# Kernel optimization log

Hardware: AMD Instinct MI355X
Metric: run time of the kernel (lower is better)

Reference implementation:

```python
import jax, jax.numpy as jnp
import numpy as np

B, T, EMB, HEAD = 8, 2048, 1024, 1024

def setup_inputs() -> dict:
    key = jax.random.key(0)
    k1, k2, k3, k4 = jax.random.split(key, 4)
    s = 1.0 / np.sqrt(EMB)
    return {
        "x": jax.random.normal(k1, (B, T, EMB), dtype=jnp.float32),
        "Wq": jax.random.normal(k2, (HEAD, EMB), dtype=jnp.float32) * s,
        "Wk": jax.random.normal(k3, (HEAD, EMB), dtype=jnp.float32) * s,
        "Wv": jax.random.normal(k4, (HEAD, EMB), dtype=jnp.float32) * s,
    }

def reference(x, Wq, Wk, Wv):
    # Bias-free projections; torch Linear weight is [out, in] -> contract on last dim.
    q = jnp.einsum('btc,hc->bth', x, Wq)  # [B,T,HEAD]
    k = jnp.einsum('btc,hc->bth', x, Wk)
    v = jnp.einsum('btc,hc->bth', x, Wv)
    C = x.shape[-1]
    scale = jnp.asarray(C, x.dtype) ** -0.5  # NOTE: scales by emb dim C, as in source
    wei = jnp.einsum('bth,bsh->bts', q, k) * scale  # [B,T,T]
    Tn = x.shape[1]
    causal = jnp.tril(jnp.ones((Tn, Tn), dtype=bool))
    wei = jnp.where(causal, wei, -jnp.inf)
    wei = jax.nn.softmax(wei, axis=-1)
    # dropout omitted (eval mode / deterministic reference)
    out = jnp.einsum('bts,bsh->bth', wei, v)  # [B,T,HEAD]
    return out
```

## Files before the change

### kernel.cpp

```cpp
#include <hip/hip_runtime.h>

typedef unsigned short u16;
typedef short short8 __attribute__((ext_vector_type(8)));
typedef float f32x4 __attribute__((ext_vector_type(4)));
typedef unsigned long long u64;

#define WS_K_OFF    33554432ULL
#define WS_PTRI     67108864ULL
#define WS_PART     104857600ULL
#define WS_NEED     105447424ULL
#define W2_K        33554432ULL
#define W2_VT       67108864ULL
#define W2_PTRI     100663296ULL
#define W2_PART     138412032ULL
#define W2_NEED     139001856ULL

__device__ __forceinline__ u16 f2bf(float f) {
    union { float f; unsigned u; } c; c.f = f;
    unsigned r = c.u + 0x7fffu + ((c.u >> 16) & 1u);
    return (u16)(r >> 16);
}
__device__ __forceinline__ float bf2f(u16 h) {
    union { unsigned u; float f; } c; c.u = ((unsigned)h) << 16; return c.f;
}
__device__ __forceinline__ void gll16(const u16* g, u16* l) {
    __builtin_amdgcn_global_load_lds(
        (const __attribute__((address_space(1))) void*)g,
        (__attribute__((address_space(3))) void*)l, 16, 0, 0);
}

template<int AMODE>
__device__ __forceinline__ void gemm_pipe(
    const u16* __restrict__ A, int lda,
    const u16* __restrict__ B, int ldb,
    int m0, int n0, int nk, u16* lds, f32x4 acc[8][4])
{
    const int tid  = threadIdx.x;
    const int lane = tid & 63;
    const int w    = tid >> 6;
    const int wm   = w >> 2, wn = w & 3;
    const int kg   = lane >> 4, l15 = lane & 15;
    const int r0   = w * 32 + (lane >> 2);
    const int s0   = (lane & 3) ^ ((r0 >> 1) & 3);

    const int ldA = AMODE ? 256 : lda;
    const u16* Ar0 = A + (size_t)(m0 + r0) * ldA + s0 * 8;
    const u16* Ar1 = Ar0 + 16 * ldA;
    const u16* Br0 = B + (size_t)(n0 + r0) * ldb + s0 * 8;
    const u16* Br1 = Br0 + 16 * ldb;

    auto aoff = [&](int t) -> int {
        return AMODE ? ((t >> 3) * 65536 + (t & 7) * 32) : t * 32;
    };
    auto STAGE = [&](int t) {
        const int ao = aoff(t), bo = t * 32, buf = (t & 3) * 16384;
        u16* dA = lds + buf + w * 1024;
        u16* dB = lds + buf + 8192 + w * 1024;
        gll16(Ar0 + ao, dA);
        gll16(Ar1 + ao, dA + 512);
        gll16(Br0 + bo, dB);
        gll16(Br1 + bo, dB + 512);
    };
    auto LDA8 = [&](short8* fa, int t) {
        const u16* h = lds + (t & 3) * 16384 + wm * 4096;
        #pragma unroll
        for (int mt = 0; mt < 8; ++mt) {
            const int row = mt * 16 + l15;
            fa[mt] = *reinterpret_cast<const short8*>(
                h + row * 32 + ((kg ^ ((row >> 1) & 3)) << 3));
        }
    };
    auto LDB4 = [&](short8* fb, int t) {
        const u16* h = lds + (t & 3) * 16384 + 8192 + wn * 2048;
        #pragma unroll
        for (int nt = 0; nt < 4; ++nt) {
            const int row = nt * 16 + l15;
            fb[nt] = *reinterpret_cast<const short8*>(
                h + row * 32 + ((kg ^ ((row >> 1) & 3)) << 3));
        }
    };
    auto MFMA32 = [&](short8* fa, short8* fb) {
        __builtin_amdgcn_s_setprio(1);
        #pragma unroll
        for (int mt = 0; mt < 8; ++mt)
            #pragma unroll
            for (int nt = 0; nt < 4; ++nt)
                acc[mt][nt] = __builtin_amdgcn_mfma_f32_16x16x32_bf16(
                    fa[mt], fb[nt], acc[mt][nt], 0, 0, 0);
        __builtin_amdgcn_s_setprio(0);
    };

    STAGE(0); STAGE(1); STAGE(2);
    asm volatile("s_waitcnt vmcnt(4)" ::: "memory");
    __builtin_amdgcn_s_barrier();

    short8 faA[8], faB[8], fb[4];
    LDA8(faA, 0);

    for (int t = 0; t < nk; t += 2) {
        LDB4(fb, t);
        LDA8(faB, t + 1);
        if (t + 3 < nk) STAGE(t + 3);
        MFMA32(faA, fb);
        if (t + 3 < nk) asm volatile("s_waitcnt vmcnt(4)" ::: "memory");
        else            asm volatile("s_waitcnt vmcnt(0)" ::: "memory");
        __builtin_amdgcn_s_barrier();

        LDB4(fb, t + 1);
        if (t + 2 < nk) LDA8(faA, t + 2);
        if (t + 4 < nk) STAGE(t + 4);
        MFMA32(faB, fb);
        if (t + 4 < nk) asm volatile("s_waitcnt vmcnt(4)" ::: "memory");
        else            asm volatile("s_waitcnt vmcnt(0)" ::: "memory");
        __builtin_amdgcn_s_barrier();
    }
}

__global__ __launch_bounds__(256) void cvt_bf16(
    const float* __restrict__ x,
    const float* __restrict__ Wq,
    const float* __restrict__ Wk,
    const float* __restrict__ Wv,
    u16* __restrict__ dst)
{
    const size_t e = ((size_t)blockIdx.x * 256 + threadIdx.x) * 8;
    const float* src;
    if (e < (size_t)16777216) {
        src = x + e;
    } else {
        size_t j = e - 16777216;
        int z = (int)(j >> 20);
        const float* Wz = (z == 0) ? Wq : (z == 1) ? Wk : Wv;
        src = Wz + (j & 1048575);
    }
    float4 a = *reinterpret_cast<const float4*>(src);
    float4 b = *reinterpret_cast<const float4*>(src + 4);
    short8 v;
    v[0] = (short)f2bf(a.x); v[1] = (short)f2bf(a.y);
    v[2] = (short)f2bf(a.z); v[3] = (short)f2bf(a.w);
    v[4] = (short)f2bf(b.x); v[5] = (short)f2bf(b.y);
    v[6] = (short)f2bf(b.z); v[7] = (short)f2bf(b.w);
    *reinterpret_cast<short8*>(dst + e) = v;
}

__global__ __launch_bounds__(512, 2) void qkv_pipe(
    const u16* __restrict__ xb, const u16* __restrict__ Wb,
    u16* __restrict__ Qo, u16* __restrict__ Ko, u16* __restrict__ VTo, int zbase)
{
    __shared__ u16 L[65536];
    const int tid = threadIdx.x, lane = tid & 63, w = tid >> 6;
    const int wm = w >> 2, wn = w & 3, kg = lane >> 4, l15 = lane & 15;
    const int m0 = blockIdx.x * 256, n0 = blockIdx.y * 256;
    const int z = blockIdx.z + zbase;

    const f32x4 z4 = {0.f, 0.f, 0.f, 0.f};
    f32x4 acc[8][4];
    #pragma unroll
    for (int i = 0; i < 8; ++i)
        #pragma unroll
        for (int j = 0; j < 4; ++j) acc[i][j] = z4;

    gemm_pipe<0>(xb, 1024, Wb + (size_t)z * 1048576, 1024, m0, n0, 32, L, acc);

    if (z < 2) {
        u16* O = (z == 0) ? Qo : Ko;
        #pragma unroll
        for (int mt = 0; mt < 8; ++mt) {
            const int row0 = m0 + wm * 128 + mt * 16 + kg * 4;
            #pragma unroll
            for (int nt = 0; nt < 4; ++nt) {
                const int col = n0 + wn * 64 + nt * 16 + l15;
                #pragma unroll
                for (int r = 0; r < 4; ++r)
                    O[(size_t)(row0 + r) * 1024 + col] = f2bf(acc[mt][nt][r]);
            }
        }
    } else {
        const int b    = m0 >> 11;
        const int mloc = m0 & 2047;
        const int t8   = (tid & 31) * 8;
        const int hh   = tid >> 5;
        #pragma unroll
        for (int half = 0; half < 2; ++half) {
            if ((wn >> 1) == half) {
                const int hb = (wn & 1) * 64;
                #pragma unroll
                for (int mt = 0; mt < 8; ++mt) {
                    const int tl = wm * 128 + mt * 16 + kg * 4;
                    #pragma unroll
                    for (int nt = 0; nt < 4; ++nt) {
                        const int hl = hb + nt * 16 + l15;
                        u64 pk = (u64)f2bf(acc[mt][nt][0])
                               | ((u64)f2bf(acc[mt][nt][1]) << 16)
                               | ((u64)f2bf(acc[mt][nt][2]) << 32)
                               | ((u64)f2bf(acc[mt][nt][3]) << 48);
                        *reinterpret_cast<u64*>(&L[hl * 264 + tl]) = pk;
                    }
                }
            }
            __syncthreads();
            #pragma unroll
            for (int p = 0; p < 8; ++p) {
                const int hl = p * 16 + hh;
                short8 v = *reinterpret_cast<const short8*>(&L[hl * 264 + t8]);
                *reinterpret_cast<short8*>(
                    &VTo[((size_t)b * 1024 + n0 + half * 128 + hl) * 2048 + mloc + t8]) = v;
            }
            __syncthreads();
        }
    }
}

template<int AMODE>
__device__ __forceinline__ void gemm_tri128(
    const u16* __restrict__ A, int lda,
    const u16* __restrict__ B, int ldb, int nk, u16* L, f32x4 acc[4][4])
{
    const int tid = threadIdx.x, lane = tid & 63, w = tid >> 6;
    const int wm = w >> 1, wn = w & 1, kg = lane >> 4, l15 = lane & 15;

    const int rA = w * 32 + (lane >> 2);
    const int sA = (lane & 3) ^ ((rA >> 1) & 3);
    const int rB = w * 16 + (lane >> 2);
    const int sB = (lane & 3) ^ ((rB >> 1) & 3);
    const int ldA = AMODE ? 256 : lda;
    const u16* Ar0 = A + (size_t)rA * ldA + sA * 8;
    const u16* Ar1 = Ar0 + 16 * ldA;
    const u16* Br0 = B + (size_t)rB * ldb + sB * 8;

    auto aoff = [&](int t) -> int {
        return AMODE ? ((t >> 3) * 65536 + (t & 7) * 32) : t * 32;
    };
    auto STAGE = [&](int t) {
        u16* d = L + (t % 3) * 12288;
        gll16(Ar0 + aoff(t), d + w * 1024);
        gll16(Ar1 + aoff(t), d + w * 1024 + 512);
        gll16(Br0 + t * 32,  d + 8192 + w * 512);
    };
    auto LDA4 = [&](short8* fa, int t) {
        const u16* h = L + (t % 3) * 12288;
        #pragma unroll
        for (int mt = 0; mt < 4; ++mt) {
            const int row = wm * 64 + mt * 16 + l15;
            fa[mt] = *reinterpret_cast<const short8*>(
                h + row * 32 + ((kg ^ ((row >> 1) & 3)) << 3));
        }
    };
    auto LDB4 = [&](short8* fb, int t) {
        const u16* h = L + (t % 3) * 12288 + 8192;
        #pragma unroll
        for (int nt = 0; nt < 4; ++nt) {
            const int row = wn * 64 + nt * 16 + l15;
            fb[nt] = *reinterpret_cast<const short8*>(
                h + row * 32 + ((kg ^ ((row >> 1) & 3)) << 3));
        }
    };

    STAGE(0); STAGE(1);
    asm volatile("s_waitcnt vmcnt(3)" ::: "memory");
    __builtin_amdgcn_s_barrier();

    short8 fa[4], fb[4];
    for (int t = 0; t < nk; ++t) {
        LDA4(fa, t);
        LDB4(fb, t);
        if (t + 2 < nk) STAGE(t + 2);
        __builtin_amdgcn_s_setprio(1);
        #pragma unroll
        for (int mt = 0; mt < 4; ++mt)
            #pragma unroll
            for (int nt = 0; nt < 4; ++nt)
                acc[mt][nt] = __builtin_amdgcn_mfma_f32_16x16x32_bf16(
                    fa[mt], fb[nt], acc[mt][nt], 0, 0, 0);
        __builtin_amdgcn_s_setprio(0);
        if (t + 2 < nk) asm volatile("s_waitcnt vmcnt(3)" ::: "memory");
        else            asm volatile("s_waitcnt vmcnt(0)" ::: "memory");
        __builtin_amdgcn_s_barrier();
    }
}

__global__ __launch_bounds__(512, 4) void sp128(
    const u16* __restrict__ Q, const u16* __restrict__ K,
    u16* __restrict__ Ptri, float* __restrict__ part)
{
    __shared__ u16 L[36864];
    int jj = blockIdx.x;
    const int b = jj / 72;
    int r = jj - b * 72;
    int qb = 0;
    while (r >= 2 * qb + 2) { r -= 2 * qb + 2; ++qb; }
    const int kb = r;

    const int tid = threadIdx.x, lane = tid & 63, w = tid >> 6;
    const int wm = w >> 1, wn = w & 1, kg = lane >> 4, l15 = lane & 15;

    const f32x4 z4 = {0.f, 0.f, 0.f, 0.f};
    f32x4 acc[4][4];
    #pragma unroll
    for (int a_ = 0; a_ < 4; ++a_)
        #pragma unroll
        for (int j = 0; j < 4; ++j) acc[a_][j] = z4;

    gemm_tri128<0>(Q + (size_t)(b * 2048 + qb * 256) * 1024, 1024,
                   K + (size_t)(b * 2048 + kb * 128) * 1024, 1024,
                   32, L, acc);

    u16* Pt = Ptri + ((size_t)b * 36 + (qb * (qb + 1)) / 2 + (kb >> 1)) * 65536
                   + (kb & 1) * 128;
    float* psum = (float*)L;
    #pragma unroll
    for (int mt = 0; mt < 4; ++mt) {
        #pragma unroll
        for (int rr = 0; rr < 4; ++rr) {
            const int lt = wm * 64 + mt * 16 + kg * 4 + rr;
            const int gt = qb * 256 + lt;
            float ps = 0.f;
            #pragma unroll
            for (int nt = 0; nt < 4; ++nt) {
                const int lcol = wn * 64 + nt * 16 + l15;
                const int gs = kb * 128 + lcol;
                const float p = (gs <= gt) ? __expf(acc[mt][nt][rr] * 0.03125f) : 0.f;
                ps += p;
                Pt[(size_t)lt * 256 + lcol] = f2bf(p);
            }
            #pragma unroll
            for (int d = 1; d < 16; d <<= 1) ps += __shfl_xor(ps, d, 64);
            if (l15 == 0) psum[lt * 2 + wn] = ps;
        }
    }
    __syncthreads();
    if (tid < 256) {
        const float s = psum[tid * 2] + psum[tid * 2 + 1];
        part[(size_t)b * 18432 + (qb * qb + qb) * 256 + tid * (2 * qb + 2) + kb] = s;
    }
}

__global__ __launch_bounds__(512, 2) void sp_old(
    const u16* __restrict__ Q, const u16* __restrict__ K, u16* __restrict__ P)
{
    const int qb = blockIdx.x, kb = blockIdx.y, b = blockIdx.z;
    if (kb > qb) return;
    __shared__ u16 L[65536];
    const int tid = threadIdx.x, lane = tid & 63, w = tid >> 6;
    const int wm = w >> 2, wn = w & 3, kg = lane >> 4, l15 = lane & 15;

    const f32x4 z4 = {0.f, 0.f, 0.f, 0.f};
    f32x4 acc[8][4];
    #pragma unroll
    for (int i = 0; i < 8; ++i)
        #pragma unroll
        for (int j = 0; j < 4; ++j) acc[i][j] = z4;

    gemm_pipe<0>(Q, 1024, K, 1024, b * 2048 + qb * 256, b * 2048 + kb * 256, 32, L, acc);

    u16* Pb = P + (size_t)b * 2048 * 2048;
    #pragma unroll
    for (int mt = 0; mt < 8; ++mt) {
        const int trow0 = qb * 256 + wm * 128 + mt * 16 + kg * 4;
        #pragma unroll
        for (int nt = 0; nt < 4; ++nt) {
            const int scol = kb * 256 + wn * 64 + nt * 16 + l15;
            #pragma unroll
            for (int r = 0; r < 4; ++r) {
                const int trow = trow0 + r;
                const float p = (scol <= trow) ? __expf(acc[mt][nt][r] * 0.03125f) : 0.f;
                Pb[(size_t)trow * 2048 + scol] = f2bf(p);
            }
        }
    }
}

__global__ __launch_bounds__(512, 4) void pv128(
    const u16* __restrict__ Ptri, const u16* __restrict__ VT,
    const float* __restrict__ part, float* __restrict__ out)
{
    __shared__ u16 L[36864];
    const int i = blockIdx.x;
    const int c = i >> 7;
    const int j = (i >> 1) & 63;
    const int s = i & 1;
    const int q  = s ? c : 7 - c;
    const int b  = j >> 3;
    const int nb = j & 7;
    const int nk = (q + 1) * 8;

    const int tid = threadIdx.x, lane = tid & 63, w = tid >> 6;
    const int wm = w >> 1, wn = w & 1, kg = lane >> 4, l15 = lane & 15;

    const f32x4 z4 = {0.f, 0.f, 0.f, 0.f};
    f32x4 acc[4][4];
    #pragma unroll
    for (int a_ = 0; a_ < 4; ++a_)
        #pragma unroll
        for (int jx = 0; jx < 4; ++jx) acc[a_][jx] = z4;

    gemm_tri128<1>(Ptri + ((size_t)b * 36 + (q * (q + 1)) / 2) * 65536, 256,
                   VT + ((size_t)b * 1024 + nb * 128) * 2048, 2048,
                   nk, L, acc);

    float* Lf = (float*)L;
    if (tid < 256) {
        const int nkb = 2 * q + 2;
        const float* pp = part + (size_t)b * 18432 + (q * q + q) * 256 + tid * nkb;
        float sum = 0.f;
        for (int kb = 0; kb < nkb; ++kb) sum += pp[kb];
        Lf[tid] = 1.f / sum;
    }
    __syncthreads();

    #pragma unroll
    for (int mt = 0; mt < 4; ++mt) {
        const int lt0 = wm * 64 + mt * 16 + kg * 4;
        const size_t grow0 = (size_t)b * 2048 + q * 256 + lt0;
        float rs[4];
        #pragma unroll
        for (int r = 0; r < 4; ++r) rs[r] = Lf[lt0 + r];
        #pragma unroll
        for (int nt = 0; nt < 4; ++nt) {
            const int col = nb * 128 + wn * 64 + nt * 16 + l15;
            #pragma unroll
            for (int r = 0; r < 4; ++r)
                out[(grow0 + r) * 1024 + col] = acc[mt][nt][r] * rs[r];
        }
    }
}

__global__ __launch_bounds__(512, 2) void pv_old(
    const u16* __restrict__ P, const u16* __restrict__ VT, float* __restrict__ Of)
{
    const int b = blockIdx.x >> 3, qblk = blockIdx.x & 7;
    const int nb = blockIdx.y;
    const int nk = (qblk + 1) * 8;
    __shared__ u16 L[65536];
    const int tid = threadIdx.x, lane = tid & 63, w = tid >> 6;
    const int wm = w >> 2, wn = w & 3, kg = lane >> 4, l15 = lane & 15;

    const f32x4 z4 = {0.f, 0.f, 0.f, 0.f};
    f32x4 acc[8][4];
    #pragma unroll
    for (int i = 0; i < 8; ++i)
        #pragma unroll
        for (int j = 0; j < 4; ++j) acc[i][j] = z4;

    gemm_pipe<0>(P + (size_t)b * 2048 * 2048, 2048,
                 VT + (size_t)b * 1024 * 2048, 2048,
                 qblk * 256, nb * 256, nk, L, acc);

    #pragma unroll
    for (int mt = 0; mt < 8; ++mt) {
        const int trow0 = qblk * 256 + wm * 128 + mt * 16 + kg * 4;
        #pragma unroll
        for (int nt = 0; nt < 4; ++nt) {
            const int col = nb * 256 + wn * 64 + nt * 16 + l15;
            #pragma unroll
            for (int r = 0; r < 4; ++r)
                Of[((size_t)b * 2048 + trow0 + r) * 1024 + col] = acc[mt][nt][r];
        }
    }
}

__global__ __launch_bounds__(256) void finalize(
    const u16* __restrict__ P, const float* __restrict__ Of, float* __restrict__ out)
{
    const int row = blockIdx.x;
    const int tid = threadIdx.x;
    const int b = row >> 11, t = row & 2047;
    const int len = ((t >> 8) + 1) * 256;
    const u16* prow = P + ((size_t)b * 2048 + t) * 2048;

    float s = 0.f;
    const int i = tid * 8;
    if (i < len) {
        short8 v = *reinterpret_cast<const short8*>(prow + i);
        #pragma unroll
        for (int j = 0; j < 8; ++j) s += bf2f((u16)v[j]);
    }
    #pragma unroll
    for (int d = 1; d < 64; d <<= 1) s += __shfl_xor(s, d, 64);

    __shared__ float red[4];
    if ((tid & 63) == 0) red[tid >> 6] = s;
    __syncthreads();
    const float rinv = 1.f / (red[0] + red[1] + red[2] + red[3]);

    const size_t o = (size_t)row * 1024 + tid * 4;
    f32x4 v = *reinterpret_cast<const f32x4*>(Of + o);
    v[0] *= rinv; v[1] *= rinv; v[2] *= rinv; v[3] *= rinv;
    *reinterpret_cast<f32x4*>(out + o) = v;
}

extern "C" void kernel_launch(void* const* d_in, const int* in_sizes, int n_in,
                              void* d_out, int out_size, void* d_ws, size_t ws_size,
                              hipStream_t stream) {
    const float* x  = (const float*)d_in[0];
    const float* Wq = (const float*)d_in[1];
    const float* Wk = (const float*)d_in[2];
    const float* Wv = (const float*)d_in[3];

    u16* xb = (u16*)d_out;
    u16* Wb = xb + (size_t)16777216;

    cvt_bf16<<<dim3(9728), 256, 0, stream>>>(x, Wq, Wk, Wv, xb);

    if (ws_size >= W2_NEED) {
        u16*   Qb   = (u16*)d_ws;
        u16*   Kb   = (u16*)((char*)d_ws + W2_K);
        u16*   VTb  = (u16*)((char*)d_ws + W2_VT);
        u16*   Pt   = (u16*)((char*)d_ws + W2_PTRI);
        float* part = (float*)((char*)d_ws + W2_PART);

        qkv_pipe<<<dim3(64, 4, 3), 512, 0, stream>>>(xb, Wb, Qb, Kb, VTb, 0);
        sp128<<<dim3(576), 512, 0, stream>>>(Qb, Kb, Pt, part);
        pv128<<<dim3(512), 512, 0, stream>>>(Pt, VTb, part, (float*)d_out);
    } else if (ws_size >= WS_NEED) {
        u16*   Qb   = (u16*)d_ws;
        u16*   Kb   = (u16*)((char*)d_ws + WS_K_OFF);
        u16*   Pt   = (u16*)((char*)d_ws + WS_PTRI);
        float* part = (float*)((char*)d_ws + WS_PART);
        u16*   VTb  = Qb;

        qkv_pipe<<<dim3(64, 4, 2), 512, 0, stream>>>(xb, Wb, Qb, Kb, Qb, 0);
        sp128<<<dim3(576), 512, 0, stream>>>(Qb, Kb, Pt, part);
        qkv_pipe<<<dim3(64, 4, 1), 512, 0, stream>>>(xb, Wb, Qb, Kb, VTb, 2);
        pv128<<<dim3(512), 512, 0, stream>>>(Pt, VTb, part, (float*)d_out);
    } else {
        u16* Qb  = (u16*)d_ws;
        u16* Kb  = Qb + (size_t)16384 * 1024;
        u16* VTb = Kb + (size_t)16384 * 1024;
        float* Of = (float*)d_ws;
        u16* Pb = (u16*)d_out;

        qkv_pipe<<<dim3(64, 4, 3), 512, 0, stream>>>(xb, Wb, Qb, Kb, VTb, 0);
        sp_old<<<dim3(8, 8, 8), 512, 0, stream>>>(Qb, Kb, Pb);
        pv_old<<<dim3(64, 4), 512, 0, stream>>>(Pb, VTb, Of);
        finalize<<<dim3(16384), 256, 0, stream>>>(Pb, Of, (float*)d_out);
    }
}
```

Baseline: 254.6 us.

## Tile causal score kernel at 128x128 blocks to skip masked upper tiles

Replaces the 256x128 score kernel with a 128x128-tile kernel that uses 256 threads and enumerates only lower-triangular 128-row blocks (136 per batch instead of 72 256-row pairs). The intent is to skip the fully masked quarter tiles that the old 256-row tiling computed, and to give the scheduler more, smaller blocks. The row-sum partials layout changes to per-128-row blocks and the PV kernel's normalization read is updated to match. The trade-off is smaller tiles with less data reuse and a different pipeline wait count.

```diff
diff --git a/kernel.cpp b/kernel.cpp
--- a/kernel.cpp
+++ b/kernel.cpp
@@ -279,21 +279,28 @@
     }
 }
 
-__global__ __launch_bounds__(512, 4) void sp128(
+__global__ __launch_bounds__(256, 3) void sp64k(
     const u16* __restrict__ Q, const u16* __restrict__ K,
     u16* __restrict__ Ptri, float* __restrict__ part)
 {
-    __shared__ u16 L[36864];
+    __shared__ u16 L[24576];
     int jj = blockIdx.x;
-    const int b = jj / 72;
-    int r = jj - b * 72;
-    int qb = 0;
-    while (r >= 2 * qb + 2) { r -= 2 * qb + 2; ++qb; }
+    const int b = jj / 136;
+    int r = jj - b * 136;
+    int q128 = 0;
+    while (r >= q128 + 1) { r -= q128 + 1; ++q128; }
     const int kb = r;
 
     const int tid = threadIdx.x, lane = tid & 63, w = tid >> 6;
     const int wm = w >> 1, wn = w & 1, kg = lane >> 4, l15 = lane & 15;
 
+    const int r0 = tid >> 2;
+    const int s0 = (tid & 3) ^ ((r0 >> 1) & 3);
+    const u16* Ar0 = Q + (size_t)(b * 2048 + q128 * 128 + r0) * 1024 + s0 * 8;
+    const u16* Ar1 = Ar0 + (size_t)64 * 1024;
+    const u16* Br0 = K + (size_t)(b * 2048 + kb * 128 + r0) * 1024 + s0 * 8;
+    const u16* Br1 = Br0 + (size_t)64 * 1024;
+
     const f32x4 z4 = {0.f, 0.f, 0.f, 0.f};
     f32x4 acc[4][4];
     #pragma unroll
@@ -301,19 +308,65 @@
         #pragma unroll
         for (int j = 0; j < 4; ++j) acc[a_][j] = z4;
 
-    gemm_tri128<0>(Q + (size_t)(b * 2048 + qb * 256) * 1024, 1024,
-                   K + (size_t)(b * 2048 + kb * 128) * 1024, 1024,
-                   32, L, acc);
-
-    u16* Pt = Ptri + ((size_t)b * 36 + (qb * (qb + 1)) / 2 + (kb >> 1)) * 65536
-                   + (kb & 1) * 128;
+    auto STAGE = [&](int t) {
+        u16* d = L + (t % 3) * 8192;
+        gll16(Ar0 + t * 32, d + w * 512);
+        gll16(Ar1 + t * 32, d + 2048 + w * 512);
+        gll16(Br0 + t * 32, d + 4096 + w * 512);
+        gll16(Br1 + t * 32, d + 4096 + 2048 + w * 512);
+    };
+    auto LDA4 = [&](short8* fa, int t) {
+        const u16* h = L + (t % 3) * 8192;
+        #pragma unroll
+        for (int mt = 0; mt < 4; ++mt) {
+            const int row = wm * 64 + mt * 16 + l15;
+            fa[mt] = *reinterpret_cast<const short8*>(
+                h + row * 32 + ((kg ^ ((row >> 1) & 3)) << 3));
+        }
+    };
+    auto LDB4 = [&](short8* fb, int t) {
+        const u16* h = L + (t % 3) * 8192 + 4096;
+        #pragma unroll
+        for (int nt = 0; nt < 4; ++nt) {
+            const int row = wn * 64 + nt * 16 + l15;
+            fb[nt] = *reinterpret_cast<const short8*>(
+                h + row * 32 + ((kg ^ ((row >> 1) & 3)) << 3));
+        }
+    };
+
+    const int nk = 32;
+    STAGE(0); STAGE(1);
+    asm volatile("s_waitcnt vmcnt(4)" ::: "memory");
+    __builtin_amdgcn_s_barrier();
+
+    short8 fa[4], fb[4];
+    for (int t = 0; t < nk; ++t) {
+        LDA4(fa, t);
+        LDB4(fb, t);
+        if (t + 2 < nk) STAGE(t + 2);
+        __builtin_amdgcn_s_setprio(1);
+        #pragma unroll
+        for (int mt = 0; mt < 4; ++mt)
+            #pragma unroll
+            for (int nt = 0; nt < 4; ++nt)
+                acc[mt][nt] = __builtin_amdgcn_mfma_f32_16x16x32_bf16(
+                    fa[mt], fb[nt], acc[mt][nt], 0, 0, 0);
+        __builtin_amdgcn_s_setprio(0);
+        if (t + 2 < nk) asm volatile("s_waitcnt vmcnt(4)" ::: "memory");
+        else            asm volatile("s_waitcnt vmcnt(0)" ::: "memory");
+        __builtin_amdgcn_s_barrier();
+    }
+
+    const int q256 = q128 >> 1, kb256 = kb >> 1;
+    u16* Pt = Ptri + ((size_t)b * 36 + (q256 * (q256 + 1)) / 2 + kb256) * 65536
+                   + (size_t)(q128 & 1) * 128 * 256 + (kb & 1) * 128;
     float* psum = (float*)L;
     #pragma unroll
     for (int mt = 0; mt < 4; ++mt) {
         #pragma unroll
         for (int rr = 0; rr < 4; ++rr) {
             const int lt = wm * 64 + mt * 16 + kg * 4 + rr;
-            const int gt = qb * 256 + lt;
+            const int gt = q128 * 128 + lt;
             float ps = 0.f;
             #pragma unroll
             for (int nt = 0; nt < 4; ++nt) {
@@ -329,9 +382,10 @@
         }
     }
     __syncthreads();
-    if (tid < 256) {
+    if (tid < 128) {
         const float s = psum[tid * 2] + psum[tid * 2 + 1];
-        part[(size_t)b * 18432 + (qb * qb + qb) * 256 + tid * (2 * qb + 2) + kb] = s;
+        part[(size_t)b * 17408 + (size_t)(q128 * (q128 + 1) / 2) * 128
+             + tid * (q128 + 1) + kb] = s;
     }
 }
 
@@ -400,10 +454,13 @@
 
     float* Lf = (float*)L;
     if (tid < 256) {
-        const int nkb = 2 * q + 2;
-        const float* pp = part + (size_t)b * 18432 + (q * q + q) * 256 + tid * nkb;
+        const int q128 = q * 2 + (tid >> 7);
+        const int rloc = tid & 127;
+        const float* pp = part + (size_t)b * 17408
+                        + (size_t)(q128 * (q128 + 1) / 2) * 128
+                        + (size_t)rloc * (q128 + 1);
         float sum = 0.f;
-        for (int kb = 0; kb < nkb; ++kb) sum += pp[kb];
+        for (int kb = 0; kb <= q128; ++kb) sum += pp[kb];
         Lf[tid] = 1.f / sum;
     }
     __syncthreads();
@@ -510,7 +567,7 @@
         float* part = (float*)((char*)d_ws + W2_PART);
 
         qkv_pipe<<<dim3(64, 4, 3), 512, 0, stream>>>(xb, Wb, Qb, Kb, VTb, 0);
-        sp128<<<dim3(576), 512, 0, stream>>>(Qb, Kb, Pt, part);
+        sp64k<<<dim3(1088), 256, 0, stream>>>(Qb, Kb, Pt, part);
         pv128<<<dim3(512), 512, 0, stream>>>(Pt, VTb, part, (float*)d_out);
     } else if (ws_size >= WS_NEED) {
         u16*   Qb   = (u16*)d_ws;
@@ -520,7 +577,7 @@
         u16*   VTb  = Qb;
 
         qkv_pipe<<<dim3(64, 4, 2), 512, 0, stream>>>(xb, Wb, Qb, Kb, Qb, 0);
-        sp128<<<dim3(576), 512, 0, stream>>>(Qb, Kb, Pt, part);
+        sp64k<<<dim3(1088), 256, 0, stream>>>(Qb, Kb, Pt, part);
         qkv_pipe<<<dim3(64, 4, 1), 512, 0, stream>>>(xb, Wb, Qb, Kb, VTb, 2);
         pv128<<<dim3(512), 512, 0, stream>>>(Pt, VTb, part, (float*)d_out);
     } else {
```

New measurement: 262.7 us. 1.03x slower.
